# Performance work log

Hardware: AMD Instinct MI355X
Metric: run time of the kernel (lower is better)

The kernel has to match this reference:

```python
import jax, jax.numpy as jnp
import numpy as np

# BitLinear (BitNet-style) constants, reconstructed from missing helpers:
#   get_qb_range(b) -> (-2^(b-1), 2^(b-1));  Qb = 2^(b-1) = 128 for bit_range=8
#   get_beta(W)  = mean(|W|)   (||W||_1 / (n*m))
#   get_gamma(W) = max(|W|)
QB = 128.0
EP = 0.01        # ep init arg: clip margin
LN_EPS = 1e-5    # nn.LayerNorm default eps
N_IN = 4096
N_OUT = 4096


def setup_inputs() -> dict:
    key = jax.random.key(0)
    kx, kw = jax.random.split(key, 2)
    x = jax.random.normal(kx, (4, 2048, N_IN), dtype=jnp.float32)
    # weight_init(): w0 ~ N(0,1); alpha = mean(w0); binarize sign(w0 - alpha)
    w0 = jax.random.normal(kw, (N_IN, N_OUT), dtype=jnp.float32)
    alpha = jnp.mean(w0)
    beta = jnp.mean(jnp.abs(w0))          # get_beta
    gamma = jnp.max(jnp.abs(w0))          # get_gamma
    w = jnp.where(w0 - alpha > 0, 1.0, -1.0).astype(jnp.float32)
    ln_gamma = jnp.ones((N_IN,), dtype=jnp.float32)   # LayerNorm weight
    ln_beta = jnp.zeros((N_IN,), dtype=jnp.float32)   # LayerNorm bias
    return {"x": x, "w": w, "ln_gamma": ln_gamma, "ln_beta": ln_beta,
            "beta": beta, "gamma": gamma}


def reference(x, w, ln_gamma, ln_beta, beta, gamma):
    # LayerNorm over last dim
    mu = jnp.mean(x, axis=-1, keepdims=True)
    var = jnp.mean(jnp.square(x - mu), axis=-1, keepdims=True)
    xn = (x - mu) * jax.lax.rsqrt(var + LN_EPS) * ln_gamma + ln_beta
    # ABSMax quantize: scale by Qb/gamma, clip to [-Qb+ep, Qb-ep] (no int cast)
    xq = jnp.clip(xn * (QB / gamma), -QB + EP, QB - EP)
    # binary-weight matmul + dequant scale beta*gamma/Qb
    y = jnp.einsum("bsi,io->bso", xq, w) * (beta * gamma / QB)
    return y
```

## Files before the change

### kernel.cpp

```cpp
#include <hip/hip_runtime.h>

using i32x4  = __attribute__((ext_vector_type(4))) int;
using i32x16 = __attribute__((ext_vector_type(16))) int;

constexpr int K_DIM = 4096;
constexpr int N_DIM = 4096;
constexpr float QBf = 128.0f;
constexpr float EPf = 0.01f;
constexpr float LN_EPSf = 1e-5f;

#define GLOAD_LDS16(gp, lp)                                                  \
    __builtin_amdgcn_global_load_lds(                                        \
        (const __attribute__((address_space(1))) void*)(gp),                 \
        (__attribute__((address_space(3))) void*)(lp), 16, 0, 0)

#define BARRIER()                                                            \
    do { asm volatile("" ::: "memory");                                      \
         __builtin_amdgcn_s_barrier();                                       \
         asm volatile("" ::: "memory"); } while (0)

#define WAIT_LGKM(N)                                                         \
    do { asm volatile("s_waitcnt lgkmcnt(" #N ")" ::: "memory");             \
         __builtin_amdgcn_sched_barrier(0); } while (0)

#define FENCE() __builtin_amdgcn_sched_barrier(0)

__global__ __launch_bounds__(256) void ln_quant_kernel(
    const float* __restrict__ x,
    const float* __restrict__ ln_g,
    const float* __restrict__ ln_b,
    const float* __restrict__ gamma_p,
    char* __restrict__ xq)
{
    const int row = blockIdx.x;
    const int t = threadIdx.x;
    const float4* xr4 = reinterpret_cast<const float4*>(x + (size_t)row * K_DIM);

    float4 v[4];
    float sum = 0.f, sumsq = 0.f;
#pragma unroll
    for (int i = 0; i < 4; ++i) {
        v[i] = xr4[t * 4 + i];
        sum += v[i].x + v[i].y + v[i].z + v[i].w;
        sumsq += v[i].x * v[i].x + v[i].y * v[i].y + v[i].z * v[i].z + v[i].w * v[i].w;
    }
#pragma unroll
    for (int off = 32; off > 0; off >>= 1) {
        sum += __shfl_down(sum, off);
        sumsq += __shfl_down(sumsq, off);
    }
    __shared__ float s_sum[4], s_sq[4];
    const int lane = t & 63, w = t >> 6;
    if (lane == 0) { s_sum[w] = sum; s_sq[w] = sumsq; }
    __syncthreads();
    sum = s_sum[0] + s_sum[1] + s_sum[2] + s_sum[3];
    sumsq = s_sq[0] + s_sq[1] + s_sq[2] + s_sq[3];

    const float mu = sum * (1.0f / K_DIM);
    const float var = sumsq * (1.0f / K_DIM) - mu * mu;
    const float rstd = rsqrtf(var + LN_EPSf);
    const float qs = QBf / gamma_p[0];
    const float lo = -QBf + EPf, hi = QBf - EPf;

    alignas(16) char ob[16];
#pragma unroll
    for (int i = 0; i < 4; ++i) {
        const float4 g = reinterpret_cast<const float4*>(ln_g)[t * 4 + i];
        const float4 b = reinterpret_cast<const float4*>(ln_b)[t * 4 + i];
        const float f0 = fminf(fmaxf(((v[i].x - mu) * rstd * g.x + b.x) * qs, lo), hi);
        const float f1 = fminf(fmaxf(((v[i].y - mu) * rstd * g.y + b.y) * qs, lo), hi);
        const float f2 = fminf(fmaxf(((v[i].z - mu) * rstd * g.z + b.z) * qs, lo), hi);
        const float f3 = fminf(fmaxf(((v[i].w - mu) * rstd * g.w + b.w) * qs, lo), hi);
        int x0 = (int)rintf(f0), x1 = (int)rintf(f1);
        int x2 = (int)rintf(f2), x3 = (int)rintf(f3);
        ob[i * 4 + 0] = (char)(x0 > 127 ? 127 : x0);
        ob[i * 4 + 1] = (char)(x1 > 127 ? 127 : x1);
        ob[i * 4 + 2] = (char)(x2 > 127 ? 127 : x2);
        ob[i * 4 + 3] = (char)(x3 > 127 ? 127 : x3);
    }
    *reinterpret_cast<uint4*>(xq + (size_t)row * K_DIM + t * 16) =
        *reinterpret_cast<const uint4*>(ob);
}

__global__ __launch_bounds__(256) void wtrans_kernel(
    const float* __restrict__ w, char* __restrict__ wq)
{
    __shared__ char tile[64][68];
    const int t = threadIdx.x;
    const int bk = blockIdx.y * 64;
    const int bn = blockIdx.x * 64;
#pragma unroll
    for (int i = 0; i < 4; ++i) {
        const int li = i * 1024 + t * 4;
        const int r = li >> 6, c = li & 63;
        const float4 vv = *reinterpret_cast<const float4*>(
            w + (size_t)(bk + r) * N_DIM + bn + c);
        tile[r][c]     = (char)vv.x;
        tile[r][c + 1] = (char)vv.y;
        tile[r][c + 2] = (char)vv.z;
        tile[r][c + 3] = (char)vv.w;
    }
    __syncthreads();
    const int n = t >> 2, kc = t & 3;
    alignas(16) char h16[16];
#pragma unroll
    for (int j = 0; j < 16; ++j) h16[j] = tile[kc * 16 + j][n];
    *reinterpret_cast<uint4*>(wq + (size_t)(bn + n) * K_DIM + bk + kc * 16) =
        *reinterpret_cast<const uint4*>(h16);
}

__global__ __launch_bounds__(512, 2) void gemm_kernel(
    const char* __restrict__ A,
    const char* __restrict__ Bt,
    float* __restrict__ C,
    const float* __restrict__ beta_p,
    const float* __restrict__ gamma_p)
{
    constexpr int NT = K_DIM / 128;
    __shared__ __align__(16) char lds[131072];

    const int t = threadIdx.x;
    const int flat = blockIdx.y * gridDim.x + blockIdx.x;
    const int xcd = flat & 7;
    const int r8 = flat >> 3;
    const int by = ((xcd >> 1) << 3) + (r8 >> 3);
    const int bx = ((xcd & 1) << 3) + (r8 & 7);
    const int bm = by * 256;
    const int bn = bx * 256;

    const int lane = t & 63;
    const int w = t >> 6;
    const int wm = w >> 2;
    const int wn = w & 3;
    const int ln31 = lane & 31;
    const int lg2 = lane >> 5;

    const char* gA = A + (size_t)bm * K_DIM;
    const char* gB = Bt + (size_t)bn * K_DIM;
    const int voff = (t & 127) * K_DIM + ((t >> 7) << 4);

    const int aoff = lg2 * 2048 + (ln31 << 4);
    const int boff = lg2 * 2048 + (((wn & 1) * 64 + ln31) << 4);

#define STAGE_OP(gbase, b, roff, kt)                                          \
    do {                                                                      \
        GLOAD_LDS16((gbase) + (size_t)(kt) * 128 + voff,                      \
                    lds + (b) * 65536 + (roff) + t * 16);                     \
        GLOAD_LDS16((gbase) + (size_t)(kt) * 128 + voff + 64,                 \
                    lds + (b) * 65536 + (roff) + 8192 + t * 16);              \
        GLOAD_LDS16((gbase) + (size_t)(128 * K_DIM) + (size_t)(kt) * 128      \
                        + voff,                                               \
                    lds + (b) * 65536 + (roff) + 16384 + t * 16);             \
        GLOAD_LDS16((gbase) + (size_t)(128 * K_DIM) + (size_t)(kt) * 128      \
                        + voff + 64,                                          \
                    lds + (b) * 65536 + (roff) + 16384 + 8192 + t * 16);      \
    } while (0)

#define STAGE_A(b, kt) STAGE_OP(gA, b, 0, kt)
#define STAGE_B(b, kt) STAGE_OP(gB, b, 32768, kt)

#define LD(p) (*reinterpret_cast<const i32x4*>(p))

#define READ_A(par, ks, mfp)                                                  \
    do {                                                                      \
        afr[par][0] = LD(ab + (ks) * 4096 + (mfp) * 1024 + aoff);             \
        afr[par][1] = LD(ab + (ks) * 4096 + (mfp) * 1024 + 512 + aoff);       \
    } while (0)

#define MFMA4(par, ks, mfp)                                                   \
    do {                                                                      \
        __builtin_amdgcn_s_setprio(1);                                        \
        _Pragma("unroll")                                                     \
        for (int m2 = 0; m2 < 2; ++m2)                                        \
            _Pragma("unroll")                                                 \
            for (int nf = 0; nf < 2; ++nf)                                    \
                acc[(mfp) * 2 + m2][nf] =                                     \
                    __builtin_amdgcn_mfma_i32_32x32x32_i8(                    \
                        afr[par][m2], bfrag[nf][ks],                          \
                        acc[(mfp) * 2 + m2][nf], 0, 0, 0);                    \
        __builtin_amdgcn_s_setprio(0);                                        \
    } while (0)

#define TILE(b, tt)                                                           \
    do {                                                                      \
        const char* ab = lds + (b) * 65536 + wm * 16384;                      \
        const char* bb = lds + (b) * 65536 + 32768 + (wn >> 1) * 16384;       \
        i32x4 bfrag[2][4];                                      \
        i32x4 afr[2][2];                                    \
        _Pragma("unroll")                                                     \
        for (int nf = 0; nf < 2; ++nf)                                        \
            _Pragma("unroll")                                                 \
            for (int ks = 0; ks < 4; ++ks)                                    \
                bfrag[nf][ks] = LD(bb + ks * 4096 + nf * 512 + boff);         \
        READ_A(0, 0, 0);                                                      \
        FENCE();                                                              \
         READ_A(1, 0, 1);                                             \
        if ((tt) + 1 < NT) STAGE_A((b) ^ 1, (tt) + 1);                        \
        WAIT_LGKM(2); MFMA4(0, 0, 0);                                         \
         READ_A(0, 1, 0); WAIT_LGKM(2); MFMA4(1, 0, 1);               \
         READ_A(1, 1, 1); WAIT_LGKM(2); MFMA4(0, 1, 0);               \
         READ_A(0, 2, 0); WAIT_LGKM(2); MFMA4(1, 1, 1);               \
        BARRIER();                                                            \
         READ_A(1, 2, 1);                                             \
        if ((tt) + 2 < NT) STAGE_B(b, (tt) + 2);                              \
        WAIT_LGKM(2); MFMA4(0, 2, 0);                                         \
         READ_A(0, 3, 0); WAIT_LGKM(2); MFMA4(1, 2, 1);               \
         READ_A(1, 3, 1); WAIT_LGKM(2); MFMA4(0, 3, 0);               \
         WAIT_LGKM(0); MFMA4(1, 3, 1);                                \
        if ((tt) + 2 < NT) asm volatile("s_waitcnt vmcnt(4)" ::: "memory");   \
        else               asm volatile("s_waitcnt vmcnt(0)" ::: "memory");   \
        BARRIER();                                                            \
    } while (0)

    i32x16 acc[4][2];
#pragma unroll
    for (int m = 0; m < 4; ++m)
#pragma unroll
        for (int n = 0; n < 2; ++n)
#pragma unroll
            for (int q = 0; q < 16; ++q)
                acc[m][n][q] = 0;

    STAGE_A(0, 0); STAGE_B(0, 0); STAGE_B(1, 1);
    asm volatile("s_waitcnt vmcnt(4)" ::: "memory");
    BARRIER();

    for (int kt = 0; kt < NT; kt += 2) {
        TILE(0, kt);
        TILE(1, kt + 1);
    }

    const float scale = beta_p[0] * gamma_p[0] * (1.0f / QBf);
    const int orow0 = bm + wm * 128 + lg2 * 4;
    const int ocol0 = bn + wn * 64 + ln31;
#pragma unroll
    for (int mf = 0; mf < 4; ++mf) {
#pragma unroll
        for (int nf = 0; nf < 2; ++nf) {
#pragma unroll
            for (int reg = 0; reg < 16; ++reg) {
                const int row = orow0 + mf * 32 + (reg & 3) + 8 * (reg >> 2);
                C[(size_t)row * N_DIM + ocol0 + nf * 32] =
                    (float)acc[mf][nf][reg] * scale;
            }
        }
    }
#undef STAGE_OP
#undef STAGE_A
#undef STAGE_B
#undef LD
#undef READ_A
#undef MFMA4
#undef TILE
}

extern "C" void kernel_launch(void* const* d_in, const int* in_sizes, int n_in,
                              void* d_out, int out_size, void* d_ws, size_t ws_size,
                              hipStream_t stream)
{
    const float* x       = (const float*)d_in[0];
    const float* w       = (const float*)d_in[1];
    const float* ln_g    = (const float*)d_in[2];
    const float* ln_b    = (const float*)d_in[3];
    const float* beta_p  = (const float*)d_in[4];
    const float* gamma_p = (const float*)d_in[5];
    float* out = (float*)d_out;

    const int M = in_sizes[0] / K_DIM;

    char* xq = (char*)d_ws;
    char* wq = (char*)d_ws + (size_t)M * K_DIM;

    ln_quant_kernel<<<M, 256, 0, stream>>>(x, ln_g, ln_b, gamma_p, xq);
    wtrans_kernel<<<dim3(N_DIM / 64, K_DIM / 64), 256, 0, stream>>>(w, wq);
    gemm_kernel<<<dim3(N_DIM / 256, M / 256), 512, 0, stream>>>(xq, wq, out, beta_p, gamma_p);
}
```

Baseline: 218.7 us.

## Triple-buffer B tiles in LDS to drop mid-tile barrier

Splits LDS into two A buffers and three B buffers (160KB) so the B prefetch for tile t+2 can be issued at the start of each tile into a free buffer. This removes the mid-tile barrier that previously guarded reuse of the B buffer, and the main loop is unrolled by six to rotate the buffer indices. The cost is more LDS per block, and 160KB of LDS may allow only one 512-thread block per CU despite launch_bounds(512,2), which would reduce occupancy.

```diff
diff --git a/kernel.cpp b/kernel.cpp
--- a/kernel.cpp
+++ b/kernel.cpp
@@ -117,7 +117,7 @@
     const float* __restrict__ gamma_p)
 {
     constexpr int NT = K_DIM / 128;
-    __shared__ __align__(16) char lds[131072];
+    __shared__ __align__(16) char lds[163840];
 
     const int t = threadIdx.x;
     const int flat = blockIdx.y * gridDim.x + blockIdx.x;
@@ -142,22 +142,22 @@
     const int aoff = lg2 * 2048 + (ln31 << 4);
     const int boff = lg2 * 2048 + (((wn & 1) * 64 + ln31) << 4);
 
-#define STAGE_OP(gbase, b, roff, kt)                                          \
+#define STAGE_OP(gbase, rbase, kt)                                            \
     do {                                                                      \
         GLOAD_LDS16((gbase) + (size_t)(kt) * 128 + voff,                      \
-                    lds + (b) * 65536 + (roff) + t * 16);                     \
+                    lds + (rbase) + t * 16);                                  \
         GLOAD_LDS16((gbase) + (size_t)(kt) * 128 + voff + 64,                 \
-                    lds + (b) * 65536 + (roff) + 8192 + t * 16);              \
+                    lds + (rbase) + 8192 + t * 16);                           \
         GLOAD_LDS16((gbase) + (size_t)(128 * K_DIM) + (size_t)(kt) * 128      \
                         + voff,                                               \
-                    lds + (b) * 65536 + (roff) + 16384 + t * 16);             \
+                    lds + (rbase) + 16384 + t * 16);                          \
         GLOAD_LDS16((gbase) + (size_t)(128 * K_DIM) + (size_t)(kt) * 128      \
                         + voff + 64,                                          \
-                    lds + (b) * 65536 + (roff) + 16384 + 8192 + t * 16);      \
-    } while (0)
-
-#define STAGE_A(b, kt) STAGE_OP(gA, b, 0, kt)
-#define STAGE_B(b, kt) STAGE_OP(gB, b, 32768, kt)
+                    lds + (rbase) + 16384 + 8192 + t * 16);                   \
+    } while (0)
+
+#define STAGE_A(abi, kt) STAGE_OP(gA, (abi) * 32768, kt)
+#define STAGE_B(bbi, kt) STAGE_OP(gB, 65536 + (bbi) * 32768, kt)
 
 #define LD(p) (*reinterpret_cast<const i32x4*>(p))
 
@@ -181,10 +181,10 @@
         __builtin_amdgcn_s_setprio(0);                                        \
     } while (0)
 
-#define TILE(b, tt)                                                           \
-    do {                                                                      \
-        const char* ab = lds + (b) * 65536 + wm * 16384;                      \
-        const char* bb = lds + (b) * 65536 + 32768 + (wn >> 1) * 16384;       \
+#define TILE(ABI, BBI, SBI, tt)                                               \
+    do {                                                                      \
+        const char* ab = lds + (ABI) * 32768 + wm * 16384;                    \
+        const char* bb = lds + 65536 + (BBI) * 32768 + (wn >> 1) * 16384;     \
         i32x4 bfrag[2][4];                                      \
         i32x4 afr[2][2];                                    \
         _Pragma("unroll")                                                     \
@@ -195,15 +195,13 @@
         READ_A(0, 0, 0);                                                      \
         FENCE();                                                              \
          READ_A(1, 0, 1);                                             \
-        if ((tt) + 1 < NT) STAGE_A((b) ^ 1, (tt) + 1);                        \
+        if ((tt) + 1 < NT) STAGE_A((ABI) ^ 1, (tt) + 1);                      \
+        if ((tt) + 2 < NT) STAGE_B(SBI, (tt) + 2);                            \
         WAIT_LGKM(2); MFMA4(0, 0, 0);                                         \
          READ_A(0, 1, 0); WAIT_LGKM(2); MFMA4(1, 0, 1);               \
          READ_A(1, 1, 1); WAIT_LGKM(2); MFMA4(0, 1, 0);               \
          READ_A(0, 2, 0); WAIT_LGKM(2); MFMA4(1, 1, 1);               \
-        BARRIER();                                                            \
-         READ_A(1, 2, 1);                                             \
-        if ((tt) + 2 < NT) STAGE_B(b, (tt) + 2);                              \
-        WAIT_LGKM(2); MFMA4(0, 2, 0);                                         \
+         READ_A(1, 2, 1); WAIT_LGKM(2); MFMA4(0, 2, 0);               \
          READ_A(0, 3, 0); WAIT_LGKM(2); MFMA4(1, 2, 1);               \
          READ_A(1, 3, 1); WAIT_LGKM(2); MFMA4(0, 3, 0);               \
          WAIT_LGKM(0); MFMA4(1, 3, 1);                                \
@@ -225,10 +223,16 @@
     asm volatile("s_waitcnt vmcnt(4)" ::: "memory");
     BARRIER();
 
-    for (int kt = 0; kt < NT; kt += 2) {
-        TILE(0, kt);
-        TILE(1, kt + 1);
-    }
+    for (int kt = 0; kt < NT - 2; kt += 6) {
+        TILE(0, 0, 2, kt);
+        TILE(1, 1, 0, kt + 1);
+        TILE(0, 2, 1, kt + 2);
+        TILE(1, 0, 2, kt + 3);
+        TILE(0, 1, 0, kt + 4);
+        TILE(1, 2, 1, kt + 5);
+    }
+    TILE(0, 0, 2, NT - 2);
+    TILE(1, 1, 0, NT - 1);
 
     const float scale = beta_p[0] * gamma_p[0] * (1.0f / QBf);
     const int orow0 = bm + wm * 128 + lg2 * 4;
```

New measurement: 226.0 us. 3.3% more time.
